# Optimization experiments

Hardware: AMD Instinct MI355X
Metric: run time of the kernel (lower is better)

Reference implementation:

```python
import jax, jax.numpy as jnp
import numpy as np

B, S, D, H = 2, 2048, 768, 12
E = D // H  # d_head = 64


def setup_inputs() -> dict:
    key = jax.random.key(0)
    ks = jax.random.split(key, 10)
    scale = 1.0 / np.sqrt(D)
    x = jax.random.normal(ks[0], (B, S, D), dtype=jnp.float32)
    # Additive mask, laid out [H*B, S, S] as the torch forward slices per head.
    attn_mask = jnp.zeros((H * B, S, S), dtype=jnp.float32)
    # Per-head projections (math form: q = x @ Wq[h] + bq[h])
    Wq = jax.random.normal(ks[1], (H, D, E), dtype=jnp.float32) * scale
    bq = jax.random.normal(ks[2], (H, E), dtype=jnp.float32) * 0.01
    Wk = jax.random.normal(ks[3], (H, D, E), dtype=jnp.float32) * scale
    bk = jax.random.normal(ks[4], (H, E), dtype=jnp.float32) * 0.01
    Wv = jax.random.normal(ks[5], (H, D, E), dtype=jnp.float32) * scale
    bv = jax.random.normal(ks[6], (H, E), dtype=jnp.float32) * 0.01
    Wo = jax.random.normal(ks[7], (D, D), dtype=jnp.float32) * scale
    bo = jax.random.normal(ks[8], (D,), dtype=jnp.float32) * 0.01
    return {"x": x, "attn_mask": attn_mask, "Wq": Wq, "bq": bq,
            "Wk": Wk, "bk": bk, "Wv": Wv, "bv": bv, "Wo": Wo, "bo": bo}


def reference(x, attn_mask, Wq, bq, Wk, bk, Wv, bv, Wo, bo):
    # x: [B,S,D]; attn_mask: [H*B,S,S]
    q = jnp.einsum('bsd,hde->hbse', x, Wq) + bq[:, None, None, :]
    k = jnp.einsum('bsd,hde->hbse', x, Wk) + bk[:, None, None, :]
    v = jnp.einsum('bsd,hde->hbse', x, Wv) + bv[:, None, None, :]
    mask = attn_mask.reshape(H, B, S, S)
    # NOTE: original code has NO 1/sqrt(d_head) scaling — kept faithful.
    logits = jnp.einsum('hbse,hbte->hbst', q, k) + mask
    w = jax.nn.softmax(logits, axis=-1)  # dropout is identity at eval / p=0
    o = jnp.einsum('hbst,hbte->hbse', w, v)  # [H,B,S,E]
    o = jnp.transpose(o, (1, 2, 0, 3)).reshape(B, S, H * E)  # concat heads
    return o @ Wo + bo
```

## Files before the change

kernel.cpp:

```cpp
#include <hip/hip_runtime.h>
#include <hip/hip_bf16.h>
#include <cmath>

constexpr int Bc  = 2;
constexpr int Sc  = 2048;
constexpr int Dc  = 768;
constexpr int Hc  = 12;
constexpr int Ec  = 64;
constexpr int BSc = Bc * Sc;

typedef _Float16 f16;
typedef __attribute__((ext_vector_type(8)))  _Float16 half8;
typedef __attribute__((ext_vector_type(16))) float    floatx16;

__global__ __launch_bounds__(256) void prep_kernel(
    const float* __restrict__ x,
    const float* __restrict__ Wq, const float* __restrict__ Wk, const float* __restrict__ Wv,
    const float* __restrict__ bq, const float* __restrict__ bk, const float* __restrict__ bv,
    const float* __restrict__ Wo,
    f16* __restrict__ x16, f16* __restrict__ Wt16, f16* __restrict__ Wot16,
    float* __restrict__ bias_cat)
{
    __shared__ __align__(16) float Ts[64][65];
    const int t = threadIdx.x;
    int bid = blockIdx.x;

    if (bid < 1536) {
        const size_t base = (size_t)bid * 2048 + t * 8;
        const float4 v0 = *(const float4*)(x + base);
        const float4 v1 = *(const float4*)(x + base + 4);
        half8 hv;
        hv[0] = (f16)v0.x; hv[1] = (f16)v0.y; hv[2] = (f16)v0.z; hv[3] = (f16)v0.w;
        hv[4] = (f16)v1.x; hv[5] = (f16)v1.y; hv[6] = (f16)v1.z; hv[7] = (f16)v1.w;
        *(half8*)(x16 + base) = hv;
        return;
    }
    bid -= 1536;
    if (bid < 432) {
        const int proj = bid / 144, rem = bid % 144, h = rem / 12, dt = rem % 12;
        const float* W = ((proj == 0) ? Wq : (proj == 1) ? Wk : Wv) + (size_t)h * Dc * Ec;
        const int c = t & 63, rr = t >> 6;
        #pragma unroll
        for (int r0 = 0; r0 < 64; r0 += 4) {
            const int d = rr + r0;
            Ts[d][c] = W[(size_t)(dt * 64 + d) * Ec + c];
        }
        __syncthreads();
        #pragma unroll
        for (int r0 = 0; r0 < 64; r0 += 4) {
            const int e = rr + r0;
            Wt16[(size_t)(proj * 768 + h * 64 + e) * Dc + dt * 64 + c] = (f16)Ts[c][e];
        }
        return;
    }
    bid -= 432;
    if (bid < 144) {
        const int rt = bid / 12, ct = bid % 12;
        const int c = t & 63, rr = t >> 6;
        #pragma unroll
        for (int r0 = 0; r0 < 64; r0 += 4) {
            const int d = rr + r0;
            Ts[d][c] = Wo[(size_t)(rt * 64 + d) * Dc + ct * 64 + c];
        }
        __syncthreads();
        #pragma unroll
        for (int r0 = 0; r0 < 64; r0 += 4) {
            const int e = rr + r0;
            Wot16[(size_t)(ct * 64 + e) * Dc + rt * 64 + c] = (f16)Ts[c][e];
        }
        return;
    }
    bid -= 144;
    {
        const int g = bid * 256 + t;
        if (g < 3 * 768) {
            const int proj = g / 768, idx = g % 768;
            const float* bb = (proj == 0) ? bq : (proj == 1) ? bk : bv;
            bias_cat[g] = bb[idx];
        }
    }
}

__global__ __launch_bounds__(256, 2) void gemm_qkv_kernel(
    const f16* __restrict__ x16, const f16* __restrict__ Wt16,
    const float* __restrict__ bias_cat,
    f16* __restrict__ q16, f16* __restrict__ k16, f16* __restrict__ v16t)
{
    __shared__ __align__(16) unsigned char smem[36864];
    f16 (*As)[72]  = (f16(*)[72])smem;
    f16 (*Bs)[72]  = (f16(*)[72])(smem + 18432);
    f16 (*Cs)[136] = (f16(*)[136])smem;

    const int t = threadIdx.x;
    const int wave = t >> 6, lane = t & 63;
    const int col = lane & 31, hf = lane >> 5;
    const int wr = wave & 1, wc = wave >> 1;
    const int m0 = blockIdx.x * 128, n0 = blockIdx.y * 128;

    floatx16 c00, c01, c10, c11;
    #pragma unroll
    for (int i = 0; i < 16; ++i) { c00[i] = 0.f; c01[i] = 0.f; c10[i] = 0.f; c11[i] = 0.f; }

    for (int k0 = 0; k0 < Dc; k0 += 64) {
        #pragma unroll
        for (int p = 0; p < 4; ++p) {
            const int cid = p * 256 + t;
            const int row = cid >> 3, seg = cid & 7;
            *(half8*)&As[row][seg * 8] =
                *(const half8*)(x16 + (size_t)(m0 + row) * Dc + k0 + seg * 8);
            *(half8*)&Bs[row][seg * 8] =
                *(const half8*)(Wt16 + (size_t)(n0 + row) * Dc + k0 + seg * 8);
        }
        __syncthreads();
        #pragma unroll
        for (int ks = 0; ks < 4; ++ks) {
            const half8 a0 = *(const half8*)&As[wr * 64 + col][ks * 16 + hf * 8];
            const half8 a1 = *(const half8*)&As[wr * 64 + 32 + col][ks * 16 + hf * 8];
            const half8 b0 = *(const half8*)&Bs[wc * 64 + col][ks * 16 + hf * 8];
            const half8 b1 = *(const half8*)&Bs[wc * 64 + 32 + col][ks * 16 + hf * 8];
            c00 = __builtin_amdgcn_mfma_f32_32x32x16_f16(a0, b0, c00, 0, 0, 0);
            c01 = __builtin_amdgcn_mfma_f32_32x32x16_f16(a0, b1, c01, 0, 0, 0);
            c10 = __builtin_amdgcn_mfma_f32_32x32x16_f16(a1, b0, c10, 0, 0, 0);
            c11 = __builtin_amdgcn_mfma_f32_32x32x16_f16(a1, b1, c11, 0, 0, 0);
        }
        __syncthreads();
    }

    const float bias0 = bias_cat[n0 + wc * 64 + col];
    const float bias1 = bias_cat[n0 + wc * 64 + 32 + col];
    #pragma unroll
    for (int i = 0; i < 16; ++i) {
        const int r = (i & 3) + 8 * (i >> 2) + 4 * hf;
        Cs[wr * 64 + r][wc * 64 + col]           = (f16)(c00[i] + bias0);
        Cs[wr * 64 + r][wc * 64 + 32 + col]      = (f16)(c01[i] + bias1);
        Cs[wr * 64 + 32 + r][wc * 64 + col]      = (f16)(c10[i] + bias0);
        Cs[wr * 64 + 32 + r][wc * 64 + 32 + col] = (f16)(c11[i] + bias1);
    }
    __syncthreads();

    const int proj = n0 / 768;
    const int h0   = (n0 - proj * 768) >> 6;
    const int b    = m0 >> 11;
    const int s_in = m0 & 2047;

    if (proj < 2) {
        f16* dst = (proj == 0) ? q16 : k16;
        const int row = t >> 1, seg = t & 1;
        const int h = h0 + seg;
        f16* gp = dst + ((size_t)(h * Bc + b) * Sc + s_in + row) * Ec;
        #pragma unroll
        for (int j = 0; j < 8; ++j)
            *(half8*)(gp + j * 8) = *(const half8*)&Cs[row][seg * 64 + j * 8];
    } else {
        const int coln = t & 127, half_ = t >> 7;
        const int seg = coln >> 6, e = coln & 63;
        const int h = h0 + seg;
        f16* gp = v16t + ((size_t)(h * Bc + b) * Ec + e) * Sc + s_in + half_ * 64;
        #pragma unroll
        for (int jb = 0; jb < 8; ++jb) {
            half8 tv;
            #pragma unroll
            for (int j2 = 0; j2 < 8; ++j2)
                tv[j2] = Cs[half_ * 64 + jb * 8 + j2][coln];
            *(half8*)(gp + jb * 8) = tv;
        }
    }
}

__global__ __launch_bounds__(256, 3) void flash_attn_kernel(
    const f16* __restrict__ q16, const f16* __restrict__ k16,
    const f16* __restrict__ v16t, const float* __restrict__ mask,
    f16* __restrict__ obuf16)
{
    __shared__ _Float16 Plds[4][32][40];
    __shared__ float Msh[2][2][32];
    __shared__ float Lsh[2][32];
    __shared__ float OLsh[2][64][33];

    const int rb   = blockIdx.x;
    const int b    = blockIdx.y;
    const int h    = blockIdx.z;
    const int hb   = h * Bc + b;
    const int t    = threadIdx.x;
    const int wave = t >> 6;
    const int lane = t & 63;
    const int rg   = wave & 1;
    const int kh   = wave >> 1;
    const int col  = lane & 31;
    const int hf   = lane >> 5;
    const int row0 = rb * 64 + rg * 32;

    const f16* qb = q16 + ((size_t)hb * Sc + row0) * Ec;
    const f16* kb = k16 + (size_t)hb * Sc * Ec;
    const f16* vb = v16t + (size_t)hb * Ec * Sc;

    half8 qfrag[4];
    #pragma unroll
    for (int ks = 0; ks < 4; ++ks)
        qfrag[ks] = *(const half8*)(qb + (size_t)col * Ec + ks * 16 + hf * 8);

    const int key_base = kh * (Sc / 2);
    constexpr int NT = (Sc / 2) / 32;

    float vmax[16];
    #pragma unroll
    for (int i = 0; i < 16; ++i) vmax[i] = -3e38f;

    for (int kt = 0; kt < NT; ++kt) {
        const int key0 = key_base + kt * 32;
        floatx16 c;
        #pragma unroll
        for (int i = 0; i < 16; ++i) c[i] = 0.f;
        #pragma unroll
        for (int ks = 0; ks < 4; ++ks) {
            const half8 kf = *(const half8*)(kb + (size_t)(key0 + col) * Ec + ks * 16 + hf * 8);
            c = __builtin_amdgcn_mfma_f32_32x32x16_f16(qfrag[ks], kf, c, 0, 0, 0);
        }
        #pragma unroll
        for (int i = 0; i < 16; ++i) vmax[i] = fmaxf(vmax[i], c[i]);
    }
    #pragma unroll
    for (int i = 0; i < 16; ++i) {
        float v = vmax[i];
        v = fmaxf(v, __shfl_xor(v, 1));
        v = fmaxf(v, __shfl_xor(v, 2));
        v = fmaxf(v, __shfl_xor(v, 4));
        v = fmaxf(v, __shfl_xor(v, 8));
        v = fmaxf(v, __shfl_xor(v, 16));
        vmax[i] = v;
    }
    if (col == 0) {
        #pragma unroll
        for (int i = 0; i < 16; ++i) {
            const int r = (i & 3) + 8 * (i >> 2) + 4 * hf;
            Msh[kh][rg][r] = vmax[i];
        }
    }
    __syncthreads();
    float mrow[16];
    #pragma unroll
    for (int i = 0; i < 16; ++i) {
        const int r = (i & 3) + 8 * (i >> 2) + 4 * hf;
        mrow[i] = fmaxf(vmax[i], Msh[1 - kh][rg][r]);
    }

    floatx16 o0, o1;
    float lsum[16];
    #pragma unroll
    for (int i = 0; i < 16; ++i) { o0[i] = 0.f; o1[i] = 0.f; lsum[i] = 0.f; }

    const float* mbase = mask + ((size_t)hb * Sc + row0) * Sc + col;

    float mbuf[16];
    #pragma unroll
    for (int i = 0; i < 16; ++i) {
        const int r = (i & 3) + 8 * (i >> 2) + 4 * hf;
        mbuf[i] = mbase[(size_t)r * Sc + key_base];
    }

    for (int kt = 0; kt < NT; ++kt) {
        const int key0 = key_base + kt * 32;

        float mcur[16];
        #pragma unroll
        for (int i = 0; i < 16; ++i) mcur[i] = mbuf[i];
        if (kt + 1 < NT) {
            #pragma unroll
            for (int i = 0; i < 16; ++i) {
                const int r = (i & 3) + 8 * (i >> 2) + 4 * hf;
                mbuf[i] = mbase[(size_t)r * Sc + key0 + 32];
            }
        }

        floatx16 c;
        #pragma unroll
        for (int i = 0; i < 16; ++i) c[i] = 0.f;
        #pragma unroll
        for (int ks = 0; ks < 4; ++ks) {
            const half8 kf = *(const half8*)(kb + (size_t)(key0 + col) * Ec + ks * 16 + hf * 8);
            c = __builtin_amdgcn_mfma_f32_32x32x16_f16(qfrag[ks], kf, c, 0, 0, 0);
        }

        #pragma unroll
        for (int i = 0; i < 16; ++i) {
            const float p = __expf(c[i] + mcur[i] - mrow[i]);
            lsum[i] += p;
            const int r = (i & 3) + 8 * (i >> 2) + 4 * hf;
            Plds[wave][r][col] = (f16)p;
        }
        asm volatile("s_waitcnt lgkmcnt(0)" ::: "memory");

        #pragma unroll
        for (int ks = 0; ks < 2; ++ks) {
            const half8 pf = *(const half8*)(&Plds[wave][col][ks * 16 + hf * 8]);
            const half8 v0 = *(const half8*)(vb + (size_t)col        * Sc + key0 + ks * 16 + hf * 8);
            const half8 v1 = *(const half8*)(vb + (size_t)(32 + col) * Sc + key0 + ks * 16 + hf * 8);
            o0 = __builtin_amdgcn_mfma_f32_32x32x16_f16(pf, v0, o0, 0, 0, 0);
            o1 = __builtin_amdgcn_mfma_f32_32x32x16_f16(pf, v1, o1, 0, 0, 0);
        }
    }

    #pragma unroll
    for (int i = 0; i < 16; ++i) {
        float v = lsum[i];
        v += __shfl_xor(v, 1);
        v += __shfl_xor(v, 2);
        v += __shfl_xor(v, 4);
        v += __shfl_xor(v, 8);
        v += __shfl_xor(v, 16);
        lsum[i] = v;
    }

    if (kh == 1) {
        if (col == 0) {
            #pragma unroll
            for (int i = 0; i < 16; ++i) {
                const int r = (i & 3) + 8 * (i >> 2) + 4 * hf;
                Lsh[rg][r] = lsum[i];
            }
        }
        #pragma unroll
        for (int i = 0; i < 16; ++i) {
            OLsh[rg][lane][i]      = o0[i];
            OLsh[rg][lane][16 + i] = o1[i];
        }
    }
    __syncthreads();
    if (kh == 0) {
        #pragma unroll
        for (int i = 0; i < 16; ++i) {
            const int r = (i & 3) + 8 * (i >> 2) + 4 * hf;
            const float inv = 1.f / (lsum[i] + Lsh[rg][r]);
            const float r0 = (o0[i] + OLsh[rg][lane][i])      * inv;
            const float r1 = (o1[i] + OLsh[rg][lane][16 + i]) * inv;
            const size_t orow = ((size_t)b * Sc + row0 + r) * Dc + h * Ec;
            obuf16[orow + col]      = (f16)r0;
            obuf16[orow + 32 + col] = (f16)r1;
        }
    }
}

__global__ __launch_bounds__(256, 2) void gemm_out_kernel(
    const f16* __restrict__ a16, const f16* __restrict__ Wot16,
    const float* __restrict__ bo, float* __restrict__ out)
{
    __shared__ __align__(16) f16 As[128][72];
    __shared__ __align__(16) f16 Bs[64][72];

    const int t = threadIdx.x;
    const int wave = t >> 6, lane = t & 63;
    const int col = lane & 31, hf = lane >> 5;
    const int m0 = blockIdx.x * 128, n0 = blockIdx.y * 64;

    floatx16 c0, c1;
    #pragma unroll
    for (int i = 0; i < 16; ++i) { c0[i] = 0.f; c1[i] = 0.f; }

    for (int k0 = 0; k0 < Dc; k0 += 64) {
        #pragma unroll
        for (int p = 0; p < 4; ++p) {
            const int cid = p * 256 + t;
            *(half8*)&As[cid >> 3][(cid & 7) * 8] =
                *(const half8*)(a16 + (size_t)(m0 + (cid >> 3)) * Dc + k0 + (cid & 7) * 8);
        }
        #pragma unroll
        for (int p = 0; p < 2; ++p) {
            const int cid = p * 256 + t;
            *(half8*)&Bs[cid >> 3][(cid & 7) * 8] =
                *(const half8*)(Wot16 + (size_t)(n0 + (cid >> 3)) * Dc + k0 + (cid & 7) * 8);
        }
        __syncthreads();
        #pragma unroll
        for (int ks = 0; ks < 4; ++ks) {
            const half8 a  = *(const half8*)&As[wave * 32 + col][ks * 16 + hf * 8];
            const half8 b0 = *(const half8*)&Bs[col][ks * 16 + hf * 8];
            const half8 b1 = *(const half8*)&Bs[32 + col][ks * 16 + hf * 8];
            c0 = __builtin_amdgcn_mfma_f32_32x32x16_f16(a, b0, c0, 0, 0, 0);
            c1 = __builtin_amdgcn_mfma_f32_32x32x16_f16(a, b1, c1, 0, 0, 0);
        }
        __syncthreads();
    }

    const float bo0 = bo[n0 + col], bo1 = bo[n0 + 32 + col];
    #pragma unroll
    for (int i = 0; i < 16; ++i) {
        const int r = (i & 3) + 8 * (i >> 2) + 4 * hf;
        const size_t ro = (size_t)(m0 + wave * 32 + r) * Dc + n0;
        out[ro + col]      = c0[i] + bo0;
        out[ro + 32 + col] = c1[i] + bo1;
    }
}

extern "C" void kernel_launch(void* const* d_in, const int* in_sizes, int n_in,
                              void* d_out, int out_size, void* d_ws, size_t ws_size,
                              hipStream_t stream)
{
    const float* x    = (const float*)d_in[0];
    const float* mask = (const float*)d_in[1];
    const float* Wq   = (const float*)d_in[2];
    const float* bq   = (const float*)d_in[3];
    const float* Wk   = (const float*)d_in[4];
    const float* bk   = (const float*)d_in[5];
    const float* Wv   = (const float*)d_in[6];
    const float* bv   = (const float*)d_in[7];
    const float* Wo   = (const float*)d_in[8];
    const float* bo   = (const float*)d_in[9];
    float* out = (float*)d_out;

    constexpr size_t NQ = (size_t)Hc * Bc * Sc * Ec;
    f16* x16    = (f16*)d_ws;
    f16* Wt16   = x16 + (size_t)BSc * Dc;
    f16* Wot16  = Wt16 + (size_t)3 * Dc * Dc;
    f16* q16    = Wot16 + (size_t)Dc * Dc;
    f16* k16    = q16 + NQ;
    f16* v16t   = k16 + NQ;
    f16* obuf16 = v16t + NQ;
    float* bias_cat = (float*)(obuf16 + NQ);

    prep_kernel<<<2121, 256, 0, stream>>>(x, Wq, Wk, Wv, bq, bk, bv, Wo,
                                          x16, Wt16, Wot16, bias_cat);

    gemm_qkv_kernel<<<dim3(BSc / 128, 2304 / 128), 256, 0, stream>>>(
        x16, Wt16, bias_cat, q16, k16, v16t);

    flash_attn_kernel<<<dim3(Sc / 64, Bc, Hc), 256, 0, stream>>>(
        q16, k16, v16t, mask, obuf16);

    gemm_out_kernel<<<dim3(BSc / 128, Dc / 64), 256, 0, stream>>>(
        obuf16, Wot16, bo, out);
}
```

Baseline: 734.4 us.

## Pre-swizzle K/V into MFMA fragment order and use direct global-to-LDS loads

The QKV GEMM epilogue now writes K and V in a fragment-major layout that matches the MFMA operand order. Each lane in the attention kernel can then fetch its K and V fragments with fully contiguous 16-byte loads instead of strided row and column reads. Both GEMMs also switch their tile staging to global_load_lds builtins, which drop the padded LDS rows and the register round trip. Removing the padding may bring back LDS bank conflicts on the MFMA fragment reads, and the V epilogue still does scalar LDS gathers.

After: 684.1 us. 1.07x faster.

```diff
diff --git a/kernel.cpp b/kernel.cpp
--- a/kernel.cpp
+++ b/kernel.cpp
@@ -12,6 +12,10 @@
 typedef _Float16 f16;
 typedef __attribute__((ext_vector_type(8)))  _Float16 half8;
 typedef __attribute__((ext_vector_type(16))) float    floatx16;
+
+typedef __attribute__((address_space(3))) void       lds_void;
+typedef __attribute__((address_space(1))) const void glb_cvoid;
+
 
 __global__ __launch_bounds__(256) void prep_kernel(
     const float* __restrict__ x,
@@ -84,11 +88,11 @@
 __global__ __launch_bounds__(256, 2) void gemm_qkv_kernel(
     const f16* __restrict__ x16, const f16* __restrict__ Wt16,
     const float* __restrict__ bias_cat,
-    f16* __restrict__ q16, f16* __restrict__ k16, f16* __restrict__ v16t)
+    f16* __restrict__ q16, f16* __restrict__ kswz, f16* __restrict__ vswz)
 {
-    __shared__ __align__(16) unsigned char smem[36864];
-    f16 (*As)[72]  = (f16(*)[72])smem;
-    f16 (*Bs)[72]  = (f16(*)[72])(smem + 18432);
+    __shared__ __align__(16) unsigned char smem[34816];
+    f16 (*As)[64]  = (f16(*)[64])smem;
+    f16 (*Bs)[64]  = (f16(*)[64])(smem + 16384);
     f16 (*Cs)[136] = (f16(*)[136])smem;
 
     const int t = threadIdx.x;
@@ -96,6 +100,7 @@
     const int col = lane & 31, hf = lane >> 5;
     const int wr = wave & 1, wc = wave >> 1;
     const int m0 = blockIdx.x * 128, n0 = blockIdx.y * 128;
+    const int lrow = lane >> 3, lseg = lane & 7;
 
     floatx16 c00, c01, c10, c11;
     #pragma unroll
@@ -103,13 +108,14 @@
 
     for (int k0 = 0; k0 < Dc; k0 += 64) {
         #pragma unroll
-        for (int p = 0; p < 4; ++p) {
-            const int cid = p * 256 + t;
-            const int row = cid >> 3, seg = cid & 7;
-            *(half8*)&As[row][seg * 8] =
-                *(const half8*)(x16 + (size_t)(m0 + row) * Dc + k0 + seg * 8);
-            *(half8*)&Bs[row][seg * 8] =
-                *(const half8*)(Wt16 + (size_t)(n0 + row) * Dc + k0 + seg * 8);
+        for (int i = 0; i < 4; ++i) {
+            const int r = wave * 32 + i * 8;
+            __builtin_amdgcn_global_load_lds(
+                (glb_cvoid*)(x16 + (size_t)(m0 + r + lrow) * Dc + k0 + lseg * 8),
+                (lds_void*)&As[r][0], 16, 0, 0);
+            __builtin_amdgcn_global_load_lds(
+                (glb_cvoid*)(Wt16 + (size_t)(n0 + r + lrow) * Dc + k0 + lseg * 8),
+                (lds_void*)&Bs[r][0], 16, 0, 0);
         }
         __syncthreads();
         #pragma unroll
@@ -142,34 +148,52 @@
     const int h0   = (n0 - proj * 768) >> 6;
     const int b    = m0 >> 11;
     const int s_in = m0 & 2047;
-
-    if (proj < 2) {
-        f16* dst = (proj == 0) ? q16 : k16;
+    const int kt0  = s_in >> 5;
+
+    if (proj == 0) {
         const int row = t >> 1, seg = t & 1;
         const int h = h0 + seg;
-        f16* gp = dst + ((size_t)(h * Bc + b) * Sc + s_in + row) * Ec;
+        f16* gp = q16 + ((size_t)(h * Bc + b) * Sc + s_in + row) * Ec;
         #pragma unroll
         for (int j = 0; j < 8; ++j)
             *(half8*)(gp + j * 8) = *(const half8*)&Cs[row][seg * 64 + j * 8];
+    } else if (proj == 1) {
+        #pragma unroll
+        for (int ch = 0; ch < 8; ++ch) {
+            const int id = ch * 256 + t;
+            const int lane_ = id & 63;
+            const int ks  = (id >> 6) & 3;
+            const int ktp = (id >> 8) & 3;
+            const int seg = (id >> 10) & 1;
+            const int colp = lane_ & 31, hfp = lane_ >> 5;
+            const int hb = (h0 + seg) * Bc + b;
+            const half8 val = *(const half8*)&Cs[ktp * 32 + colp][seg * 64 + ks * 16 + hfp * 8];
+            *(half8*)(kswz + ((size_t)((hb * 64 + kt0 + ktp) * 4 + ks) << 9) + lane_ * 8) = val;
+        }
     } else {
-        const int coln = t & 127, half_ = t >> 7;
-        const int seg = coln >> 6, e = coln & 63;
-        const int h = h0 + seg;
-        f16* gp = v16t + ((size_t)(h * Bc + b) * Ec + e) * Sc + s_in + half_ * 64;
-        #pragma unroll
-        for (int jb = 0; jb < 8; ++jb) {
-            half8 tv;
+        #pragma unroll
+        for (int ch = 0; ch < 8; ++ch) {
+            const int id = ch * 256 + t;
+            const int lane_ = id & 63;
+            const int ks2 = (id >> 6) & 1;
+            const int vh  = (id >> 7) & 1;
+            const int ktp = (id >> 8) & 3;
+            const int seg = (id >> 10) & 1;
+            const int colp = lane_ & 31, hfp = lane_ >> 5;
+            const int hb = (h0 + seg) * Bc + b;
+            const int e  = vh * 32 + colp;
+            half8 val;
             #pragma unroll
-            for (int j2 = 0; j2 < 8; ++j2)
-                tv[j2] = Cs[half_ * 64 + jb * 8 + j2][coln];
-            *(half8*)(gp + jb * 8) = tv;
+            for (int j = 0; j < 8; ++j)
+                val[j] = Cs[ktp * 32 + ks2 * 16 + hfp * 8 + j][seg * 64 + e];
+            *(half8*)(vswz + ((size_t)(((hb * 64 + kt0 + ktp) * 2 + ks2) * 2 + vh) << 9) + lane_ * 8) = val;
         }
     }
 }
 
 __global__ __launch_bounds__(256, 3) void flash_attn_kernel(
-    const f16* __restrict__ q16, const f16* __restrict__ k16,
-    const f16* __restrict__ v16t, const float* __restrict__ mask,
+    const f16* __restrict__ q16, const f16* __restrict__ kswz,
+    const f16* __restrict__ vswz, const float* __restrict__ mask,
     f16* __restrict__ obuf16)
 {
     __shared__ _Float16 Plds[4][32][40];
@@ -190,16 +214,15 @@
     const int hf   = lane >> 5;
     const int row0 = rb * 64 + rg * 32;
 
-    const f16* qb = q16 + ((size_t)hb * Sc + row0) * Ec;
-    const f16* kb = k16 + (size_t)hb * Sc * Ec;
-    const f16* vb = v16t + (size_t)hb * Ec * Sc;
+    const f16* qb  = q16  + ((size_t)hb * Sc + row0) * Ec;
+    const f16* kbz = kswz + ((size_t)hb << 17);
+    const f16* vbz = vswz + ((size_t)hb << 17);
 
     half8 qfrag[4];
     #pragma unroll
     for (int ks = 0; ks < 4; ++ks)
         qfrag[ks] = *(const half8*)(qb + (size_t)col * Ec + ks * 16 + hf * 8);
 
-    const int key_base = kh * (Sc / 2);
     constexpr int NT = (Sc / 2) / 32;
 
     float vmax[16];
@@ -207,13 +230,14 @@
     for (int i = 0; i < 16; ++i) vmax[i] = -3e38f;
 
     for (int kt = 0; kt < NT; ++kt) {
-        const int key0 = key_base + kt * 32;
+        const int ktg = kh * NT + kt;
+        const f16* kp = kbz + ((size_t)ktg << 11) + lane * 8;
         floatx16 c;
         #pragma unroll
         for (int i = 0; i < 16; ++i) c[i] = 0.f;
         #pragma unroll
         for (int ks = 0; ks < 4; ++ks) {
-            const half8 kf = *(const half8*)(kb + (size_t)(key0 + col) * Ec + ks * 16 + hf * 8);
+            const half8 kf = *(const half8*)(kp + (ks << 9));
             c = __builtin_amdgcn_mfma_f32_32x32x16_f16(qfrag[ks], kf, c, 0, 0, 0);
         }
         #pragma unroll
@@ -250,6 +274,7 @@
     for (int i = 0; i < 16; ++i) { o0[i] = 0.f; o1[i] = 0.f; lsum[i] = 0.f; }
 
     const float* mbase = mask + ((size_t)hb * Sc + row0) * Sc + col;
+    const int key_base = kh * (Sc / 2);
 
     float mbuf[16];
     #pragma unroll
@@ -259,6 +284,7 @@
     }
 
     for (int kt = 0; kt < NT; ++kt) {
+        const int ktg  = kh * NT + kt;
         const int key0 = key_base + kt * 32;
 
         float mcur[16];
@@ -272,12 +298,13 @@
             }
         }
 
+        const f16* kp = kbz + ((size_t)ktg << 11) + lane * 8;
         floatx16 c;
         #pragma unroll
         for (int i = 0; i < 16; ++i) c[i] = 0.f;
         #pragma unroll
         for (int ks = 0; ks < 4; ++ks) {
-            const half8 kf = *(const half8*)(kb + (size_t)(key0 + col) * Ec + ks * 16 + hf * 8);
+            const half8 kf = *(const half8*)(kp + (ks << 9));
             c = __builtin_amdgcn_mfma_f32_32x32x16_f16(qfrag[ks], kf, c, 0, 0, 0);
         }
 
@@ -290,11 +317,12 @@
         }
         asm volatile("s_waitcnt lgkmcnt(0)" ::: "memory");
 
-        #pragma unroll
-        for (int ks = 0; ks < 2; ++ks) {
-            const half8 pf = *(const half8*)(&Plds[wave][col][ks * 16 + hf * 8]);
-            const half8 v0 = *(const half8*)(vb + (size_t)col        * Sc + key0 + ks * 16 + hf * 8);
-            const half8 v1 = *(const half8*)(vb + (size_t)(32 + col) * Sc + key0 + ks * 16 + hf * 8);
+        const f16* vp = vbz + ((size_t)ktg << 11) + lane * 8;
+        #pragma unroll
+        for (int ks2 = 0; ks2 < 2; ++ks2) {
+            const half8 pf = *(const half8*)(&Plds[wave][col][ks2 * 16 + hf * 8]);
+            const half8 v0 = *(const half8*)(vp + ((ks2 * 2 + 0) << 9));
+            const half8 v1 = *(const half8*)(vp + ((ks2 * 2 + 1) << 9));
             o0 = __builtin_amdgcn_mfma_f32_32x32x16_f16(pf, v0, o0, 0, 0, 0);
             o1 = __builtin_amdgcn_mfma_f32_32x32x16_f16(pf, v1, o1, 0, 0, 0);
         }
@@ -344,13 +372,14 @@
     const f16* __restrict__ a16, const f16* __restrict__ Wot16,
     const float* __restrict__ bo, float* __restrict__ out)
 {
-    __shared__ __align__(16) f16 As[128][72];
-    __shared__ __align__(16) f16 Bs[64][72];
+    __shared__ __align__(16) f16 As[128][64];
+    __shared__ __align__(16) f16 Bs[64][64];
 
     const int t = threadIdx.x;
     const int wave = t >> 6, lane = t & 63;
     const int col = lane & 31, hf = lane >> 5;
     const int m0 = blockIdx.x * 128, n0 = blockIdx.y * 64;
+    const int lrow = lane >> 3, lseg = lane & 7;
 
     floatx16 c0, c1;
     #pragma unroll
@@ -358,16 +387,20 @@
 
     for (int k0 = 0; k0 < Dc; k0 += 64) {
         #pragma unroll
-        for (int p = 0; p < 4; ++p) {
-            const int cid = p * 256 + t;
-            *(half8*)&As[cid >> 3][(cid & 7) * 8] =
-                *(const half8*)(a16 + (size_t)(m0 + (cid >> 3)) * Dc + k0 + (cid & 7) * 8);
-        }
-        #pragma unroll
-        for (int p = 0; p < 2; ++p) {
-            const int cid = p * 256 + t;
-            *(half8*)&Bs[cid >> 3][(cid & 7) * 8] =
-                *(const half8*)(Wot16 + (size_t)(n0 + (cid >> 3)) * Dc + k0 + (cid & 7) * 8);
+        for (int i = 0; i < 4; ++i) {
+            const int r = wave * 32 + i * 8;
+            __builtin_amdgcn_global_load_lds(
+                (glb_cvoid*)(a16 + (size_t)(m0 + r + lrow) * Dc + k0 + lseg * 8),
+                (lds_void*)&As[r][0], 16, 0, 0);
+        }
+        {
+            const int r = wave * 16;
+            __builtin_amdgcn_global_load_lds(
+                (glb_cvoid*)(Wot16 + (size_t)(n0 + r + lrow) * Dc + k0 + lseg * 8),
+                (lds_void*)&Bs[r][0], 16, 0, 0);
+            __builtin_amdgcn_global_load_lds(
+                (glb_cvoid*)(Wot16 + (size_t)(n0 + r + 8 + lrow) * Dc + k0 + lseg * 8),
+                (lds_void*)&Bs[r + 8][0], 16, 0, 0);
         }
         __syncthreads();
         #pragma unroll
@@ -412,19 +445,19 @@
     f16* Wt16   = x16 + (size_t)BSc * Dc;
     f16* Wot16  = Wt16 + (size_t)3 * Dc * Dc;
     f16* q16    = Wot16 + (size_t)Dc * Dc;
-    f16* k16    = q16 + NQ;
-    f16* v16t   = k16 + NQ;
-    f16* obuf16 = v16t + NQ;
+    f16* kswz   = q16 + NQ;
+    f16* vswz   = kswz + NQ;
+    f16* obuf16 = vswz + NQ;
     float* bias_cat = (float*)(obuf16 + NQ);
 
     prep_kernel<<<2121, 256, 0, stream>>>(x, Wq, Wk, Wv, bq, bk, bv, Wo,
                                           x16, Wt16, Wot16, bias_cat);
 
     gemm_qkv_kernel<<<dim3(BSc / 128, 2304 / 128), 256, 0, stream>>>(
-        x16, Wt16, bias_cat, q16, k16, v16t);
+        x16, Wt16, bias_cat, q16, kswz, vswz);
 
     flash_attn_kernel<<<dim3(Sc / 64, Bc, Hc), 256, 0, stream>>>(
-        q16, k16, v16t, mask, obuf16);
+        q16, kswz, vswz, mask, obuf16);
 
     gemm_out_kernel<<<dim3(BSc / 128, Dc / 64), 256, 0, stream>>>(
         obuf16, Wot16, bo, out);
```
